# Kernel optimization log

Hardware: AMD Instinct MI355X
Metric: run time of the kernel (lower is better)

## Reference

```python
import jax, jax.numpy as jnp
import numpy as np
import math

B, S, D, H = 4, 1024, 1024, 16
DK = D // H  # 64


def setup_inputs() -> dict:
    key = jax.random.key(0)
    ks = jax.random.split(key, 16)
    inp = {
        "query": jax.random.normal(ks[0], (B, S, D), dtype=jnp.float32),
        "key": jax.random.normal(ks[1], (B, S, D), dtype=jnp.float32),
        "value": jax.random.normal(ks[2], (B, S, D), dtype=jnp.float32),
        "mask": jax.random.randint(ks[3], (B, 1, S, S), 0, 2, dtype=jnp.int32),
        "relation_bias_matrix": jax.random.normal(ks[4], (S, S, DK), dtype=jnp.float32),
    }
    # learned params: 3 input projections + output projection (nn.Linear d_model->d_model)
    sc = 1.0 / math.sqrt(D)
    for i, nm in enumerate(["Wq", "Wk", "Wv", "Wo"]):
        inp[nm] = jax.random.normal(ks[5 + i], (D, D), dtype=jnp.float32) * sc
    for i, nm in enumerate(["bq", "bk", "bv", "bo"]):
        inp[nm] = jax.random.normal(ks[9 + i], (D,), dtype=jnp.float32) * sc
    return inp


def reference(query, key, value, mask, relation_bias_matrix,
              Wq, bq, Wk, bk, Wv, bv, Wo, bo):
    b, s, d = query.shape
    h, dk = H, DK
    scale = 1.0 / math.sqrt(dk)

    def proj(x, W, bias):
        # [B,S,D] -> [B,H,S,dk]
        return (x @ W + bias).reshape(b, s, h, dk).transpose(0, 2, 1, 3)

    q = proj(query, Wq, bq)
    k = proj(key, Wk, bk)
    v = proj(value, Wv, bv)

    # NOTE: source scales score1 by 1/sqrt(dk), then scales (score1+score2) again.
    score1 = jnp.einsum('bhid,bhjd->bhij', q, k) * scale
    # relation bias: rel[i,j,:] is a d_k key for (query pos i, key pos j)
    score2 = jnp.einsum('bhid,ijd->bhij', q, relation_bias_matrix)
    scores = (score1 + score2) * scale
    scores = jnp.where(mask == 0, jnp.asarray(-1e9, scores.dtype), scores)
    p_attn = jax.nn.softmax(scores, axis=-1)  # dropout p=0.0 -> identity
    x = jnp.einsum('bhij,bhjd->bhid', p_attn, v)
    x = x.transpose(0, 2, 1, 3).reshape(b, s, d)
    return x @ Wo + bo
```

## Files before the change

kernel.cpp:

```cpp
#include <hip/hip_runtime.h>
#include <hip/hip_bf16.h>


typedef unsigned short u16;
typedef unsigned int u32;
typedef unsigned long long u64;
typedef __attribute__((ext_vector_type(8))) short bf16x8;
typedef __attribute__((ext_vector_type(4))) float f32x4;

#define SB 1024
#define DM 1024
#define NHD 16
#define DKH 64
#define NBATCH 4

#define PIN() do { __builtin_amdgcn_sched_barrier(0); asm volatile("" ::: "memory"); } while (0)

__device__ __forceinline__ u16 f2bf(float x) {
  union { __hip_bfloat16 b; u16 u; } c;
  c.b = __float2bfloat16(x);
  return c.u;
}

__device__ __forceinline__ f32x4 mfma16(bf16x8 a, bf16x8 b, f32x4 c) {
  return __builtin_amdgcn_mfma_f32_16x16x32_bf16(a, b, c, 0, 0, 0);
}

__device__ __forceinline__ bf16x8 cvt8r(float4 v0, float4 v1) {
  bf16x8 r;
  r[0] = (short)f2bf(v0.x); r[1] = (short)f2bf(v0.y);
  r[2] = (short)f2bf(v0.z); r[3] = (short)f2bf(v0.w);
  r[4] = (short)f2bf(v1.x); r[5] = (short)f2bf(v1.y);
  r[6] = (short)f2bf(v1.z); r[7] = (short)f2bf(v1.w);
  return r;
}

__global__ void ra_convert_in(const float* __restrict__ q, const float* __restrict__ k,
                              const float* __restrict__ v,
                              u16* __restrict__ Xq, u16* __restrict__ Xk, u16* __restrict__ Xv)
{
  const int z = blockIdx.y;
  const float* src = (z == 0) ? q : (z == 1) ? k : v;
  u16* dst = (z == 0) ? Xq : (z == 1) ? Xk : Xv;
  const int n4 = NBATCH * SB * DM / 4;
  int idx = blockIdx.x * blockDim.x + threadIdx.x;
  int stride = gridDim.x * blockDim.x;
  for (int i = idx; i < n4; i += stride) {
    float4 v4 = *((const float4*)src + i);
    uint2 o;
    o.x = (u32)f2bf(v4.x) | ((u32)f2bf(v4.y) << 16);
    o.y = (u32)f2bf(v4.z) | ((u32)f2bf(v4.w) << 16);
    *((uint2*)dst + i) = o;
  }
}

__global__ void ra_transpose_w(const float* __restrict__ Wq, const float* __restrict__ Wk,
                               const float* __restrict__ Wv, const float* __restrict__ Wo,
                               u16* __restrict__ WqT, u16* __restrict__ WkT,
                               u16* __restrict__ WvT, u16* __restrict__ WoT)
{
  const int z = blockIdx.z;
  const float* W = (z == 0) ? Wq : (z == 1) ? Wk : (z == 2) ? Wv : Wo;
  u16* WT = (z == 0) ? WqT : (z == 1) ? WkT : (z == 2) ? WvT : WoT;
  __shared__ float tile[32][33];
  const int x0 = blockIdx.x * 32, y0 = blockIdx.y * 32;
  const int tx = threadIdx.x, ty = threadIdx.y;
#pragma unroll
  for (int yy = 0; yy < 4; ++yy) {
    int r = ty + yy * 8;
    tile[r][tx] = W[(size_t)(y0 + r) * DM + x0 + tx];
  }
  __syncthreads();
#pragma unroll
  for (int yy = 0; yy < 4; ++yy) {
    int r = ty + yy * 8;
    WT[(size_t)(x0 + r) * DM + y0 + tx] = f2bf(tile[tx][r]);
  }
}

__device__ __forceinline__ void gemm_core_128(const u16* __restrict__ A, const u16* __restrict__ Bt,
                                              int bm0, int bn0, u16* sh, f32x4 (&acc)[4][4])
{
  u16* As = sh;
  u16* Bs = sh + 128 * 72;
  const int tid = threadIdx.x;
  const int lane = tid & 63, wid = tid >> 6;
  const int l15 = lane & 15, l4 = lane >> 4;
  const int wr = (wid >> 1) * 64, wc = (wid & 1) * 64;
  for (int k0 = 0; k0 < DM; k0 += 64) {
#pragma unroll
    for (int it = 0; it < 4; ++it) {
      int c = tid + it * 256;
      int rw = c >> 3, kc = c & 7;
      *(uint4*)(As + rw * 72 + kc * 8) = *(const uint4*)(A + (size_t)(bm0 + rw) * DM + k0 + kc * 8);
      *(uint4*)(Bs + rw * 72 + kc * 8) = *(const uint4*)(Bt + (size_t)(bn0 + rw) * DM + k0 + kc * 8);
    }
    __syncthreads();
#pragma unroll
    for (int kf = 0; kf < 2; ++kf) {
      bf16x8 a[4], b[4];
#pragma unroll
      for (int mf = 0; mf < 4; ++mf)
        a[mf] = *(const bf16x8*)(As + (wr + mf * 16 + l15) * 72 + kf * 32 + l4 * 8);
#pragma unroll
      for (int nf = 0; nf < 4; ++nf)
        b[nf] = *(const bf16x8*)(Bs + (wc + nf * 16 + l15) * 72 + kf * 32 + l4 * 8);
#pragma unroll
      for (int mf = 0; mf < 4; ++mf)
#pragma unroll
        for (int nf = 0; nf < 4; ++nf)
          acc[mf][nf] = mfma16(a[mf], b[nf], acc[mf][nf]);
    }
    __syncthreads();
  }
}

__global__ __launch_bounds__(256, 2)
void ra_proj_gemm(const u16* __restrict__ Xq, const u16* __restrict__ Xk, const u16* __restrict__ Xv,
                  const u16* __restrict__ WqT, const u16* __restrict__ WkT, const u16* __restrict__ WvT,
                  const float* __restrict__ bq, const float* __restrict__ bk, const float* __restrict__ bv,
                  u16* __restrict__ q_ws, u16* __restrict__ k_ws, u16* __restrict__ vT_ws)
{
  __shared__ alignas(16) u16 sh[128 * 72 * 2];
  const int mode = blockIdx.z;
  const u16* A  = (mode == 0) ? Xq : (mode == 1) ? Xk : Xv;
  const u16* Bt = (mode == 0) ? WqT : (mode == 1) ? WkT : WvT;
  const float* bias = (mode == 0) ? bq : (mode == 1) ? bk : bv;
  const int bm0 = blockIdx.x * 128, bn0 = blockIdx.y * 128;
  f32x4 acc[4][4] = {};
  gemm_core_128(A, Bt, bm0, bn0, sh, acc);
  const int tid = threadIdx.x;
  const int lane = tid & 63, wid = tid >> 6;
  const int l15 = lane & 15, l4 = lane >> 4;
  const int wr = (wid >> 1) * 64, wc = (wid & 1) * 64;
  const int b_idx = bm0 >> 10;
  const int srow0 = bm0 & (SB - 1);
  if (mode < 2) {
    u16* outp = (mode == 0) ? q_ws : k_ws;
#pragma unroll
    for (int nf = 0; nf < 4; ++nf) {
      int nn = bn0 + wc + nf * 16 + l15;
      float bv_ = bias[nn];
      int h = nn >> 6, d = nn & 63;
#pragma unroll
      for (int mf = 0; mf < 4; ++mf)
#pragma unroll
        for (int r = 0; r < 4; ++r) {
          int m = wr + mf * 16 + l4 * 4 + r;
          outp[((size_t)(b_idx * NHD + h) * SB + srow0 + m) * DKH + d] = f2bf(acc[mf][nf][r] + bv_);
        }
    }
  } else {
    u16* ct = sh;
#pragma unroll
    for (int nf = 0; nf < 4; ++nf) {
      int nl = wc + nf * 16 + l15;
      float bv_ = bias[bn0 + nl];
#pragma unroll
      for (int mf = 0; mf < 4; ++mf)
#pragma unroll
        for (int r = 0; r < 4; ++r) {
          int m = wr + mf * 16 + l4 * 4 + r;
          ct[nl * 136 + m] = f2bf(acc[mf][nf][r] + bv_);
        }
    }
    __syncthreads();
#pragma unroll
    for (int it = 0; it < 8; ++it) {
      int c = tid + it * 256;
      int n = c >> 4, mc2 = c & 15;
      uint4 v = *(const uint4*)(ct + n * 136 + mc2 * 8);
      int nn = bn0 + n;
      int h = nn >> 6, d = nn & 63;
      *(uint4*)(vT_ws + ((size_t)(b_idx * NHD + h) * DKH + d) * SB + srow0 + mc2 * 8) = v;
    }
  }
}

__global__ __launch_bounds__(256, 2)
void ra_out_gemm(const u16* __restrict__ X, const u16* __restrict__ WoT,
                 const float* __restrict__ bo, float* __restrict__ out)
{
  __shared__ alignas(16) u16 sh[128 * 72 * 2];
  const int bm0 = blockIdx.x * 128, bn0 = blockIdx.y * 128;
  f32x4 acc[4][4] = {};
  gemm_core_128(X, WoT, bm0, bn0, sh, acc);
  const int tid = threadIdx.x;
  const int lane = tid & 63, wid = tid >> 6;
  const int l15 = lane & 15, l4 = lane >> 4;
  const int wr = (wid >> 1) * 64, wc = (wid & 1) * 64;
#pragma unroll
  for (int nf = 0; nf < 4; ++nf) {
    int nn = bn0 + wc + nf * 16 + l15;
    float bv_ = bo[nn];
#pragma unroll
    for (int mf = 0; mf < 4; ++mf)
#pragma unroll
      for (int r = 0; r < 4; ++r) {
        int m = wr + mf * 16 + l4 * 4 + r;
        out[(size_t)(bm0 + m) * DM + nn] = acc[mf][nf][r] + bv_;
      }
  }
}

__global__ __launch_bounds__(256)
void ra_mask_pack(const int* __restrict__ mask, u32* __restrict__ mb)
{
  const size_t t = (size_t)blockIdx.x * 256 + threadIdx.x;
  const int lane = threadIdx.x & 63;
  u64 b = __ballot(mask[t] != 0);
  if (lane == 0) *(u64*)(mb + (t >> 6) * 2) = b;
}

__global__ __launch_bounds__(1024, 1)
void ra_attn(const u16* __restrict__ q_ws, const u16* __restrict__ k_ws,
             const u16* __restrict__ vT_ws, const u32* __restrict__ mb,
             const float* __restrict__ rel, u16* __restrict__ x_ws)
{
  __shared__ _Float16 s2t[2][16 * 292 + 8];

  const int tid = threadIdx.x, wid = tid >> 6, lane = tid & 63;
  const int l15 = lane & 15, l4 = lane >> 4;
  const int g = blockIdx.y, i0 = blockIdx.x * 16;
  const int bh_g = g * NHD + wid;
  const float scl1 = 0.125f, scl2 = 0.015625f;

  bf16x8 q1[2], q2[2];
#pragma unroll
  for (int kf = 0; kf < 2; ++kf) {
    q1[kf] = *(const bf16x8*)(q_ws + ((size_t)bh_g * SB + i0 + l15) * DKH + kf * 32 + l4 * 8);
    q2[kf] = *(const bf16x8*)(q_ws + ((size_t)(g * NHD + l15) * SB + i0 + wid) * DKH + kf * 32 + l4 * 8);
  }

  bf16x8 ka[2];
  float4 rr[4];
  uint2  vb2[4];
  u32    mw;

  const u16* kbase = k_ws + (size_t)bh_g * SB * DKH;
  const u16* vbase = vT_ws + (size_t)bh_g * DKH * SB;
  const float* rbase = rel + (size_t)(i0 + wid) * SB * DKH;
  const u32* mbase = mb + ((size_t)g * SB + i0 + l15) * 32;

#pragma unroll
  for (int kf = 0; kf < 2; ++kf)
    ka[kf] = *(const bf16x8*)(kbase + (size_t)l15 * DKH + kf * 32 + l4 * 8);
  {
    const float* rp = rbase + (size_t)l15 * DKH + l4 * 8;
    rr[0] = *(const float4*)rp;       rr[1] = *(const float4*)(rp + 4);
    rr[2] = *(const float4*)(rp + 32); rr[3] = *(const float4*)(rp + 36);
  }
#pragma unroll
  for (int df = 0; df < 4; ++df)
    vb2[df] = *(const uint2*)(vbase + (size_t)(df * 16 + l15) * SB + l4 * 4);
  mw = mbase[0];
  PIN();

  f32x4 acc_o[4] = {};
  float m_run = -1e30f, l_run = 0.f;

  for (int jt = 0; jt < 64; ++jt) {
    const int jb = jt * 16;
    const int jbn = (jt < 63) ? jb + 16 : jb;
    const int cur = jt & 1;

    {
      bf16x8 rb0 = cvt8r(rr[0], rr[1]);
      bf16x8 rb1 = cvt8r(rr[2], rr[3]);
      f32x4 t = {};
      t = mfma16(rb0, q2[0], t);
      t = mfma16(rb1, q2[1], t);
      union { _Float16 h[4]; uint2 u; } w;
#pragma unroll
      for (int r = 0; r < 4; ++r) w.h[r] = (_Float16)(t[r] * scl1);
      *(uint2*)&s2t[cur][wid * 292 + l15 * 18 + l4 * 4] = w.u;
    }
    {
      const float* rp = rbase + (size_t)(jbn + l15) * DKH + l4 * 8;
      rr[0] = *(const float4*)rp;       rr[1] = *(const float4*)(rp + 4);
      rr[2] = *(const float4*)(rp + 32); rr[3] = *(const float4*)(rp + 36);
    }
    PIN();

    f32x4 sc1 = {};
    sc1 = mfma16(ka[0], q1[0], sc1);
    sc1 = mfma16(ka[1], q1[1], sc1);
#pragma unroll
    for (int kf = 0; kf < 2; ++kf)
      ka[kf] = *(const bf16x8*)(kbase + (size_t)(jbn + l15) * DKH + kf * 32 + l4 * 8);
    PIN();

    __syncthreads();

    float fsc;
    bf16x8 pa;
    {
      uint2 s2u = *(const uint2*)&s2t[cur][l15 * 292 + wid * 18 + l4 * 4];
      union { uint2 u; _Float16 h[4]; } s2c; s2c.u = s2u;
      const int mbit = (jt & 1) * 16 + l4 * 4;
      float sv[4];
#pragma unroll
      for (int r = 0; r < 4; ++r) {
        float v = sc1[r] * scl2 + (float)s2c.h[r];
        sv[r] = ((mw >> (mbit + r)) & 1u) ? v : -1e9f;
      }
      float tmax = fmaxf(fmaxf(sv[0], sv[1]), fmaxf(sv[2], sv[3]));
      tmax = fmaxf(tmax, __shfl_xor(tmax, 16));
      tmax = fmaxf(tmax, __shfl_xor(tmax, 32));
      const float m_new = fmaxf(m_run, tmax);
      fsc = __expf(m_run - m_new);
      float p0 = __expf(sv[0] - m_new), p1 = __expf(sv[1] - m_new);
      float p2 = __expf(sv[2] - m_new), p3 = __expf(sv[3] - m_new);
      float psum = p0 + p1 + p2 + p3;
      psum += __shfl_xor(psum, 16);
      psum += __shfl_xor(psum, 32);
      l_run = l_run * fsc + psum;
      m_run = m_new;
      union { bf16x8 v; u32 w[4]; } pk;
      pk.w[0] = (u32)f2bf(p0) | ((u32)f2bf(p1) << 16);
      pk.w[1] = (u32)f2bf(p2) | ((u32)f2bf(p3) << 16);
      pk.w[2] = 0; pk.w[3] = 0;
      pa = pk.v;
    }

#pragma unroll
    for (int df = 0; df < 4; ++df) {
      union { bf16x8 v; uint2 q[2]; } vv;
      vv.q[0] = vb2[df];
      vv.q[1] = make_uint2(0, 0);
      f32x4 c = acc_o[df];
      c[0] *= fsc; c[1] *= fsc; c[2] *= fsc; c[3] *= fsc;
      acc_o[df] = mfma16(vv.v, pa, c);
    }
#pragma unroll
    for (int df = 0; df < 4; ++df)
      vb2[df] = *(const uint2*)(vbase + (size_t)(df * 16 + l15) * SB + jbn + l4 * 4);
    mw = mbase[(jt + 1 < 64) ? ((jt + 1) >> 1) : 31];
    PIN();
  }

  const float inv = 1.f / l_run;
#pragma unroll
  for (int df = 0; df < 4; ++df) {
    union { u16 h[4]; uint2 u; } o;
#pragma unroll
    for (int r = 0; r < 4; ++r) o.h[r] = f2bf(acc_o[df][r] * inv);
    *(uint2*)(x_ws + ((size_t)g * SB + i0 + l15) * DM + wid * DKH + df * 16 + l4 * 4) = o.u;
  }
}

extern "C" void kernel_launch(void* const* d_in, const int* in_sizes, int n_in,
                              void* d_out, int out_size, void* d_ws, size_t ws_size,
                              hipStream_t stream) {
  const float* query = (const float*)d_in[0];
  const float* key_  = (const float*)d_in[1];
  const float* value = (const float*)d_in[2];
  const int*   mask  = (const int*)d_in[3];
  const float* rel   = (const float*)d_in[4];
  const float* Wq = (const float*)d_in[5];
  const float* Wk = (const float*)d_in[6];
  const float* Wv = (const float*)d_in[7];
  const float* Wo = (const float*)d_in[8];
  const float* bq = (const float*)d_in[9];
  const float* bk = (const float*)d_in[10];
  const float* bv = (const float*)d_in[11];
  const float* bo = (const float*)d_in[12];
  float* out = (float*)d_out;
  char* ws = (char*)d_ws;

  u16* Xq   = (u16*)(ws + (0ull));
  u16* Xk   = (u16*)(ws + (8ull << 20));
  u16* Xv   = (u16*)(ws + (16ull << 20));
  u16* WqT  = (u16*)(ws + (24ull << 20));
  u16* WkT  = (u16*)(ws + (26ull << 20));
  u16* WvT  = (u16*)(ws + (28ull << 20));
  u16* WoT  = (u16*)(ws + (30ull << 20));
  u16* q_ws = (u16*)(ws + (32ull << 20));
  u16* k_ws = (u16*)(ws + (40ull << 20));
  u16* vT_ws= (u16*)(ws + (48ull << 20));
  u16* x_ws = (u16*)(ws + (56ull << 20));
  u32* mb   = (u32*)(ws + (16ull << 20));

  ra_convert_in<<<dim3(1024, 3), 256, 0, stream>>>(query, key_, value, Xq, Xk, Xv);
  ra_transpose_w<<<dim3(32, 32, 4), dim3(32, 8), 0, stream>>>(Wq, Wk, Wv, Wo, WqT, WkT, WvT, WoT);
  ra_proj_gemm<<<dim3(32, 8, 3), 256, 0, stream>>>(Xq, Xk, Xv, WqT, WkT, WvT, bq, bk, bv,
                                                   q_ws, k_ws, vT_ws);
  ra_mask_pack<<<16384, 256, 0, stream>>>(mask, mb);
  ra_attn<<<dim3(64, 4), 1024, 0, stream>>>(q_ws, k_ws, vT_ws, mb, rel, x_ws);
  ra_out_gemm<<<dim3(32, 8), 256, 0, stream>>>(x_ws, WoT, bo, out);
}
```

Baseline: 422.5 us.

## Unroll attention loop by two tiles with deeper prefetch and lazy softmax rescale

The attention loop is manually unrolled two tiles per iteration, with separate K and relation-bias register buffers so each load is issued two tiles ahead. The __syncthreads is replaced by an explicit lgkmcnt wait plus s_barrier, and the memory clobber is dropped from the schedule pin. Online softmax now rescales the accumulators only when the new tile max exceeds the running max by more than a threshold, which skips most exp and multiply work per tile. This raises register pressure, and the lazy-rescale threshold allows intermediate values up to exp(8) before renormalising.

```diff
diff --git a/kernel.cpp b/kernel.cpp
--- a/kernel.cpp
+++ b/kernel.cpp
@@ -14,7 +14,7 @@
 #define DKH 64
 #define NBATCH 4
 
-#define PIN() do { __builtin_amdgcn_sched_barrier(0); asm volatile("" ::: "memory"); } while (0)
+#define PIN() __builtin_amdgcn_sched_barrier(0)
 
 __device__ __forceinline__ u16 f2bf(float x) {
   union { __hip_bfloat16 b; u16 u; } c;
@@ -232,23 +232,28 @@
     q2[kf] = *(const bf16x8*)(q_ws + ((size_t)(g * NHD + l15) * SB + i0 + wid) * DKH + kf * 32 + l4 * 8);
   }
 
-  bf16x8 ka[2];
-  float4 rr[4];
-  uint2  vb2[4];
-  u32    mw;
-
   const u16* kbase = k_ws + (size_t)bh_g * SB * DKH;
   const u16* vbase = vT_ws + (size_t)bh_g * DKH * SB;
   const float* rbase = rel + (size_t)(i0 + wid) * SB * DKH;
   const u32* mbase = mb + ((size_t)g * SB + i0 + l15) * 32;
 
-#pragma unroll
-  for (int kf = 0; kf < 2; ++kf)
-    ka[kf] = *(const bf16x8*)(kbase + (size_t)l15 * DKH + kf * 32 + l4 * 8);
+  bf16x8 kaA[2], kaB[2];
+  float4 rrA[4], rrB[4];
+  uint2  vb2[4];
+  u32    mw;
+
+#pragma unroll
+  for (int kf = 0; kf < 2; ++kf) {
+    kaA[kf] = *(const bf16x8*)(kbase + (size_t)l15 * DKH + kf * 32 + l4 * 8);
+    kaB[kf] = *(const bf16x8*)(kbase + (size_t)(16 + l15) * DKH + kf * 32 + l4 * 8);
+  }
   {
     const float* rp = rbase + (size_t)l15 * DKH + l4 * 8;
-    rr[0] = *(const float4*)rp;       rr[1] = *(const float4*)(rp + 4);
-    rr[2] = *(const float4*)(rp + 32); rr[3] = *(const float4*)(rp + 36);
+    rrA[0] = *(const float4*)rp;        rrA[1] = *(const float4*)(rp + 4);
+    rrA[2] = *(const float4*)(rp + 32); rrA[3] = *(const float4*)(rp + 36);
+    const float* rp2 = rbase + (size_t)(16 + l15) * DKH + l4 * 8;
+    rrB[0] = *(const float4*)rp2;        rrB[1] = *(const float4*)(rp2 + 4);
+    rrB[2] = *(const float4*)(rp2 + 32); rrB[3] = *(const float4*)(rp2 + 36);
   }
 #pragma unroll
   for (int df = 0; df < 4; ++df)
@@ -259,85 +264,95 @@
   f32x4 acc_o[4] = {};
   float m_run = -1e30f, l_run = 0.f;
 
-  for (int jt = 0; jt < 64; ++jt) {
-    const int jb = jt * 16;
-    const int jbn = (jt < 63) ? jb + 16 : jb;
-    const int cur = jt & 1;
-
-    {
-      bf16x8 rb0 = cvt8r(rr[0], rr[1]);
-      bf16x8 rb1 = cvt8r(rr[2], rr[3]);
-      f32x4 t = {};
-      t = mfma16(rb0, q2[0], t);
-      t = mfma16(rb1, q2[1], t);
-      union { _Float16 h[4]; uint2 u; } w;
-#pragma unroll
-      for (int r = 0; r < 4; ++r) w.h[r] = (_Float16)(t[r] * scl1);
-      *(uint2*)&s2t[cur][wid * 292 + l15 * 18 + l4 * 4] = w.u;
-    }
-    {
-      const float* rp = rbase + (size_t)(jbn + l15) * DKH + l4 * 8;
-      rr[0] = *(const float4*)rp;       rr[1] = *(const float4*)(rp + 4);
-      rr[2] = *(const float4*)(rp + 32); rr[3] = *(const float4*)(rp + 36);
-    }
-    PIN();
-
-    f32x4 sc1 = {};
-    sc1 = mfma16(ka[0], q1[0], sc1);
-    sc1 = mfma16(ka[1], q1[1], sc1);
-#pragma unroll
-    for (int kf = 0; kf < 2; ++kf)
-      ka[kf] = *(const bf16x8*)(kbase + (size_t)(jbn + l15) * DKH + kf * 32 + l4 * 8);
-    PIN();
-
-    __syncthreads();
-
-    float fsc;
-    bf16x8 pa;
-    {
-      uint2 s2u = *(const uint2*)&s2t[cur][l15 * 292 + wid * 18 + l4 * 4];
-      union { uint2 u; _Float16 h[4]; } s2c; s2c.u = s2u;
-      const int mbit = (jt & 1) * 16 + l4 * 4;
-      float sv[4];
-#pragma unroll
-      for (int r = 0; r < 4; ++r) {
-        float v = sc1[r] * scl2 + (float)s2c.h[r];
-        sv[r] = ((mw >> (mbit + r)) & 1u) ? v : -1e9f;
-      }
-      float tmax = fmaxf(fmaxf(sv[0], sv[1]), fmaxf(sv[2], sv[3]));
-      tmax = fmaxf(tmax, __shfl_xor(tmax, 16));
-      tmax = fmaxf(tmax, __shfl_xor(tmax, 32));
-      const float m_new = fmaxf(m_run, tmax);
-      fsc = __expf(m_run - m_new);
-      float p0 = __expf(sv[0] - m_new), p1 = __expf(sv[1] - m_new);
-      float p2 = __expf(sv[2] - m_new), p3 = __expf(sv[3] - m_new);
-      float psum = p0 + p1 + p2 + p3;
-      psum += __shfl_xor(psum, 16);
-      psum += __shfl_xor(psum, 32);
-      l_run = l_run * fsc + psum;
-      m_run = m_new;
-      union { bf16x8 v; u32 w[4]; } pk;
-      pk.w[0] = (u32)f2bf(p0) | ((u32)f2bf(p1) << 16);
-      pk.w[1] = (u32)f2bf(p2) | ((u32)f2bf(p3) << 16);
-      pk.w[2] = 0; pk.w[3] = 0;
-      pa = pk.v;
-    }
-
-#pragma unroll
-    for (int df = 0; df < 4; ++df) {
-      union { bf16x8 v; uint2 q[2]; } vv;
-      vv.q[0] = vb2[df];
-      vv.q[1] = make_uint2(0, 0);
-      f32x4 c = acc_o[df];
-      c[0] *= fsc; c[1] *= fsc; c[2] *= fsc; c[3] *= fsc;
-      acc_o[df] = mfma16(vv.v, pa, c);
-    }
-#pragma unroll
-    for (int df = 0; df < 4; ++df)
-      vb2[df] = *(const uint2*)(vbase + (size_t)(df * 16 + l15) * SB + jbn + l4 * 4);
-    mw = mbase[(jt + 1 < 64) ? ((jt + 1) >> 1) : 31];
-    PIN();
-  }
+#define TILE_BODY(RR, KA, BUF, MSHIFT, TPK, TPV)                                      \
+  {                                                                                   \
+                      \
+    bf16x8 rb0 = cvt8r(RR[0], RR[1]);                                                 \
+    bf16x8 rb1 = cvt8r(RR[2], RR[3]);                                                 \
+    f32x4 t2 = {};                                                                    \
+    t2 = mfma16(rb0, q2[0], t2);                                                      \
+    t2 = mfma16(rb1, q2[1], t2);                                                      \
+    union { _Float16 h[4]; uint2 u; } w2;                                             \
+    _Pragma("unroll") for (int r = 0; r < 4; ++r) w2.h[r] = (_Float16)(t2[r] * scl1); \
+    *(uint2*)&s2t[BUF][wid * 292 + l15 * 18 + l4 * 4] = w2.u;                         \
+                                         \
+    {                                                                                 \
+      const float* rp = rbase + (size_t)((TPK) * 16 + l15) * DKH + l4 * 8;            \
+      RR[0] = *(const float4*)rp;        RR[1] = *(const float4*)(rp + 4);            \
+      RR[2] = *(const float4*)(rp + 32); RR[3] = *(const float4*)(rp + 36);           \
+    }                                                                                 \
+    PIN();                                                                            \
+                                      \
+    f32x4 sc1 = {};                                                                   \
+    sc1 = mfma16(KA[0], q1[0], sc1);                                                  \
+    sc1 = mfma16(KA[1], q1[1], sc1);                                                  \
+                                                           \
+    KA[0] = *(const bf16x8*)(kbase + (size_t)((TPK) * 16 + l15) * DKH + l4 * 8);      \
+    KA[1] = *(const bf16x8*)(kbase + (size_t)((TPK) * 16 + l15) * DKH + 32 + l4 * 8); \
+    PIN();                                                                            \
+        \
+    asm volatile("s_waitcnt lgkmcnt(0)");                                             \
+    __builtin_amdgcn_sched_barrier(0);                                                \
+    __builtin_amdgcn_s_barrier();                                                     \
+    __builtin_amdgcn_sched_barrier(0);                                                \
+    {                                                                                 \
+      uint2 s2u = *(const uint2*)&s2t[BUF][l15 * 292 + wid * 18 + l4 * 4];            \
+      union { uint2 u; _Float16 h[4]; } s2c; s2c.u = s2u;                             \
+      float sv0 = sc1[0] * scl2 + (float)s2c.h[0];                                    \
+      float sv1 = sc1[1] * scl2 + (float)s2c.h[1];                                    \
+      float sv2 = sc1[2] * scl2 + (float)s2c.h[2];                                    \
+      float sv3 = sc1[3] * scl2 + (float)s2c.h[3];                                    \
+      const u32 mbits = mw >> (MSHIFT);                                               \
+      sv0 = (mbits & 1u) ? sv0 : -1e9f;                                               \
+      sv1 = (mbits & 2u) ? sv1 : -1e9f;                                               \
+      sv2 = (mbits & 4u) ? sv2 : -1e9f;                                               \
+      sv3 = (mbits & 8u) ? sv3 : -1e9f;                                               \
+      float tmax = fmaxf(fmaxf(sv0, sv1), fmaxf(sv2, sv3));                           \
+      if (!__all(tmax <= m_run + 8.0f)) {                      \
+        float rmax = fmaxf(tmax, __shfl_xor(tmax, 16));                               \
+        rmax = fmaxf(rmax, __shfl_xor(rmax, 32));                                     \
+        float m_new = fmaxf(m_run, rmax);                                             \
+        float fsc = __expf(m_run - m_new);                                            \
+        l_run *= fsc; m_run = m_new;                                                  \
+        _Pragma("unroll") for (int df = 0; df < 4; ++df) {                            \
+          acc_o[df][0] *= fsc; acc_o[df][1] *= fsc;                                   \
+          acc_o[df][2] *= fsc; acc_o[df][3] *= fsc;                                   \
+        }                                                                             \
+      }                                                                               \
+      float p0 = __expf(sv0 - m_run), p1 = __expf(sv1 - m_run);                       \
+      float p2 = __expf(sv2 - m_run), p3 = __expf(sv3 - m_run);                       \
+      float psum = (p0 + p1) + (p2 + p3);                                             \
+      psum += __shfl_xor(psum, 16);                                                   \
+      psum += __shfl_xor(psum, 32);                                                   \
+      l_run += psum;                                                                  \
+      union { bf16x8 v; u32 w[4]; } pk;                                               \
+      pk.w[0] = (u32)f2bf(p0) | ((u32)f2bf(p1) << 16);                                \
+      pk.w[1] = (u32)f2bf(p2) | ((u32)f2bf(p3) << 16);                                \
+      pk.w[2] = 0; pk.w[3] = 0;                                                       \
+             \
+      _Pragma("unroll") for (int df = 0; df < 4; ++df) {                              \
+        union { bf16x8 v; uint2 q[2]; } vv;                                           \
+        vv.q[0] = vb2[df];                                                            \
+        vv.q[1] = make_uint2(0, 0);                                                   \
+        acc_o[df] = mfma16(vv.v, pk.v, acc_o[df]);                                    \
+      }                                                                               \
+    }                                                                                 \
+                                                        \
+    _Pragma("unroll") for (int df = 0; df < 4; ++df)                                  \
+      vb2[df] = *(const uint2*)(vbase + (size_t)(df * 16 + l15) * SB + (TPV) * 16 + l4 * 4); \
+    PIN();                                                                            \
+  }
+
+  for (int t = 0; t < 32; ++t) {
+    const int tpA = (2 * t + 2 < 64) ? 2 * t + 2 : 63;
+    const int tpB = (2 * t + 3 < 64) ? 2 * t + 3 : 63;
+    const int tvB = (2 * t + 2 < 64) ? 2 * t + 2 : 63;
+    TILE_BODY(rrA, kaA, 0, (l4 * 4), tpA, (2 * t + 1));
+    const u32 mwN = mbase[(t + 1 < 32) ? (t + 1) : 31];
+    TILE_BODY(rrB, kaB, 1, (16 + l4 * 4), tpB, tvB);
+    mw = mwN;
+  }
+#undef TILE_BODY
 
   const float inv = 1.f / l_run;
 #pragma unroll
```

Measured after the change: 539.2 us. 1.28x slower.
